# Kernel optimization log

Hardware: AMD Instinct MI355X
Metric: run time of the kernel (lower is better)

The kernel has to match this reference:

```python
import jax, jax.numpy as jnp
import numpy as np

TAU = 1.0
EPS = 1e-8  # F.cosine_similarity eps


def _cl(X, Y):
    # Pairwise cosine similarity via L2-normalize + single GEMM (N,D)@(D,N)
    Xn = X / jnp.maximum(jnp.linalg.norm(X, axis=1, keepdims=True), EPS)
    Yn = Y / jnp.maximum(jnp.linalg.norm(Y, axis=1, keepdims=True), EPS)
    sim = Xn @ Yn.T  # [N, N], sim[i, j] = cos(X_i, Y_j)
    e = jnp.exp(sim / TAU)
    pos = jnp.diagonal(e)               # exp(diag(sim)/tau), [N]
    neg = jnp.sum(e, axis=0) - pos      # column sums minus positive, [N]
    return -jnp.log(pos / neg).reshape(X.shape[0], 1)


def setup_inputs() -> dict:
    key = jax.random.key(0)
    ks = jax.random.split(key, 6)
    N, D1, D2, DO = 8192, 1024, 768, 256
    X = jax.random.normal(ks[0], (N, D1), dtype=jnp.float32)
    Y = jax.random.normal(ks[1], (N, D2), dtype=jnp.float32)
    # nn.Linear params (kaiming-uniform-ish scale)
    Wx = jax.random.uniform(ks[2], (DO, D1), jnp.float32, -1, 1) / np.sqrt(D1)
    bx = jax.random.uniform(ks[3], (DO,), jnp.float32, -1, 1) / np.sqrt(D1)
    Wy = jax.random.uniform(ks[4], (DO, D2), jnp.float32, -1, 1) / np.sqrt(D2)
    by = jax.random.uniform(ks[5], (DO,), jnp.float32, -1, 1) / np.sqrt(D2)
    return {"X": X, "Y": Y, "Wx": Wx, "bx": bx, "Wy": Wy, "by": by}


def reference(X, Y, Wx, bx, Wy, by):
    Xp = X @ Wx.T + bx  # proj_x
    Yp = Y @ Wy.T + by  # proj_y
    return _cl(Xp, Yp) + _cl(Yp, Xp)  # [N, 1]
```

## Files before the change

kernel.cpp:

```cpp
#include <hip/hip_runtime.h>
#include <hip/hip_bf16.h>

typedef __bf16 bf16_t;
typedef __bf16 bf16x8 __attribute__((ext_vector_type(8)));
typedef float  f32x4  __attribute__((ext_vector_type(4)));
typedef unsigned long u64;
typedef u64 u64x2 __attribute__((ext_vector_type(2)));

__device__ __forceinline__ bf16x8 pack8(f32x4 a, f32x4 b) {
    bf16x8 h = { (bf16_t)a.x, (bf16_t)a.y, (bf16_t)a.z, (bf16_t)a.w,
                 (bf16_t)b.x, (bf16_t)b.y, (bf16_t)b.z, (bf16_t)b.w };
    return h;
}

__device__ __forceinline__ void gl_lds16(const void* g, void* l) {
    __builtin_amdgcn_global_load_lds(
        (const __attribute__((address_space(1))) unsigned int*)g,
        (__attribute__((address_space(3))) unsigned int*)l, 16, 0, 0);
}

#if __has_builtin(__builtin_amdgcn_cvt_pk_fp8_f32)
__device__ __forceinline__ unsigned char cvt1_e4m3(float x) {
    return (unsigned char)(__builtin_amdgcn_cvt_pk_fp8_f32(x, x, 0, false) & 0xff);
}
#else
__device__ __forceinline__ unsigned char cvt1_e4m3(float x) {
    unsigned u = __float_as_uint(x);
    unsigned sign = (u >> 24) & 0x80u;
    float a = fabsf(x);
    if (a < 7.8125e-3f) { int q = (int)(a * 512.0f + 0.5f); return (unsigned char)(sign | q); }
    if (a >= 448.0f) return (unsigned char)(sign | 0x7E);
    unsigned au = u & 0x7FFFFFFFu;
    unsigned lsb = (au >> 20) & 1u;
    au += 0x7FFFFu + lsb;
    int exp = (int)(au >> 23) - 127;
    unsigned man = (au >> 20) & 7u;
    return (unsigned char)(sign | ((unsigned)(exp + 7) << 3) | man);
}
#endif

__device__ __forceinline__ int frag_off_k(int row16, int k) {
    return ((k >> 6) << 10) + (((k >> 3) & 3) << 8) + (row16 << 4)
         + (((k >> 5) & 1) << 3) + (k & 7);
}

__global__ __launch_bounds__(256) void wconv(
    const float* __restrict__ Wx, const float* __restrict__ Wy,
    bf16_t* __restrict__ Wxt, bf16_t* __restrict__ Wyt,
    float* __restrict__ sums)
{
    int id = blockIdx.x * 256 + threadIdx.x;
    if (blockIdx.x < 64) sums[id] = 0.0f;

    int row, k0, K;
    const float* W;
    bf16_t* Wt;
    if (id < 32768) { W = Wx; Wt = Wxt; K = 1024; row = id >> 7; k0 = (id & 127) << 3; }
    else { int c = id - 32768; W = Wy; Wt = Wyt; K = 768; row = c / 96; k0 = (c % 96) << 3; }

    f32x4 lo = *reinterpret_cast<const f32x4*>(&W[(size_t)row * K + k0]);
    f32x4 hi = *reinterpret_cast<const f32x4*>(&W[(size_t)row * K + k0 + 4]);
    size_t off = (size_t)(row >> 4) * 16 * K + frag_off_k(row & 15, k0);
    *reinterpret_cast<bf16x8*>(Wt + off) = pack8(lo, hi);
}

__global__ __launch_bounds__(512, 2) void proj_norm(
    const float* __restrict__ X, const float* __restrict__ Y,
    const bf16_t* __restrict__ Wxt, const float* __restrict__ bxp,
    const bf16_t* __restrict__ Wyt, const float* __restrict__ byp,
    unsigned char* __restrict__ Xt, unsigned char* __restrict__ Yt)
{
    __shared__ float Abuf[2][64 * 64];
    __shared__ unsigned char obuf[16384];
    __shared__ float ssq2[4][2][16];

    const int tid   = threadIdx.x;
    const int lane  = tid & 63;
    const int wave  = tid >> 6;
    const int quad  = lane >> 4;
    const int c16   = lane & 15;
    const int strip = wave >> 1;
    const int half  = wave & 1;

    const bool isY = blockIdx.x >= 128;
    const float*  A    = isY ? Y   : X;
    const bf16_t* Wt   = isY ? Wyt : Wxt;
    const float*  bias = isY ? byp : bxp;
    unsigned char* dst = isY ? Yt  : Xt;
    const int K = isY ? 768 : 1024;
    const int S = K >> 6;
    const int rowBase = (blockIdx.x & 127) * 64;

    auto stage = [&](int s, int b) {
        #pragma unroll
        for (int t = 0; t < 2; ++t) {
            int r0  = (wave * 2 + t) * 4;
            int row = r0 + (lane >> 4);
            int gch = (lane & 15) ^ (row & 15);
            gl_lds16(&A[(size_t)(rowBase + row) * K + s * 64 + gch * 4],
                     &Abuf[b][r0 * 64]);
        }
    };

    auto aFrag = [&](int b, int s2) -> bf16x8 {
        int row = strip * 16 + c16;
        int e   = s2 * 8 + quad * 2;
        const float* base = &Abuf[b][row * 64];
        f32x4 lo = *reinterpret_cast<const f32x4*>(base + ((e ^ c16) << 2));
        f32x4 hi = *reinterpret_cast<const f32x4*>(base + (((e + 1) ^ c16) << 2));
        return pack8(lo, hi);
    };

    const bf16_t* pB = Wt + (size_t)(half * 8) * 16 * K + quad * 256 + c16 * 16;
    const size_t tStride = (size_t)16 * K;

    f32x4 acc[8] = {};
    stage(0, 0);

    for (int s = 0; s < S; ++s) {
        const int b = s & 1;
        __syncthreads();
        if (s + 1 < S) stage(s + 1, b ^ 1);
        #pragma unroll
        for (int s2 = 0; s2 < 2; ++s2) {
            bf16x8 aF = aFrag(b, s2);
            #pragma unroll
            for (int nf = 0; nf < 8; ++nf) {
                bf16x8 bF = *reinterpret_cast<const bf16x8*>(
                    pB + (size_t)nf * tStride + s * 1024 + s2 * 8);
                acc[nf] = __builtin_amdgcn_mfma_f32_16x16x32_bf16(aF, bF, acc[nf], 0, 0, 0);
            }
        }
    }

    #pragma unroll
    for (int nf = 0; nf < 8; ++nf) {
        float bb = bias[half * 128 + nf * 16 + c16];
        #pragma unroll
        for (int r = 0; r < 4; ++r) acc[nf][r] += bb;
    }

    #pragma unroll
    for (int r = 0; r < 4; ++r) {
        float v = 0.f;
        #pragma unroll
        for (int nf = 0; nf < 8; ++nf) v += acc[nf][r] * acc[nf][r];
        v += __shfl_xor(v, 1, 64);
        v += __shfl_xor(v, 2, 64);
        v += __shfl_xor(v, 4, 64);
        v += __shfl_xor(v, 8, 64);
        if (c16 == 0) ssq2[strip][half][quad * 4 + r] = v;
    }
    __syncthreads();

    #pragma unroll
    for (int r = 0; r < 4; ++r) {
        int row16 = quad * 4 + r;
        float t = ssq2[strip][0][row16] + ssq2[strip][1][row16];
        float inv = 1.0f / fmaxf(sqrtf(t), 1e-8f);
        #pragma unroll
        for (int nf = 0; nf < 8; ++nf) {
            int k = half * 128 + nf * 16 + c16;
            obuf[strip * 4096 + frag_off_k(row16, k)] = cvt1_e4m3(acc[nf][r] * inv);
        }
    }
    __syncthreads();

    const f32x4* src = reinterpret_cast<const f32x4*>(&obuf[tid * 32]);
    f32x4* g = reinterpret_cast<f32x4*>(dst + (size_t)rowBase * 256 + tid * 32);
    g[0] = src[0];
    g[1] = src[1];
}

__global__ __launch_bounds__(256) void sim_gemm(
    const unsigned char* __restrict__ Xt, const unsigned char* __restrict__ Yt,
    float* __restrict__ rowsum, float* __restrict__ colsum,
    float* __restrict__ pos)
{
    __shared__ float red[256];

    const int tid  = threadIdx.x;
    const int lane = tid & 63;
    const int wave = tid >> 6;
    const int quad = lane >> 4;
    const int c16  = lane & 15;
    const int wy   = wave >> 1;
    const int wx   = wave & 1;
    const int rowBase = blockIdx.x * 128;
    const int colBase = blockIdx.y * 128;

    const u64x2* pa[4];
    const u64x2* pb[4];
    #pragma unroll
    for (int mf = 0; mf < 4; ++mf)
        pa[mf] = reinterpret_cast<const u64x2*>(
            Xt + (size_t)(rowBase + wy * 64 + mf * 16) * 256 + quad * 256 + c16 * 16);
    #pragma unroll
    for (int nf = 0; nf < 4; ++nf)
        pb[nf] = reinterpret_cast<const u64x2*>(
            Yt + (size_t)(colBase + wx * 64 + nf * 16) * 256 + quad * 256 + c16 * 16);

    f32x4 acc[4][4] = {};

    auto loadf = [&](u64x2* A, u64x2* B, int slab) {
        #pragma unroll
        for (int i = 0; i < 4; ++i) {
            A[i] = pa[i][slab * 64];
            B[i] = pb[i][slab * 64];
        }
    };
    auto mm = [&](const u64x2* A, const u64x2* B) {
        #pragma unroll
        for (int mf = 0; mf < 4; ++mf)
            #pragma unroll
            for (int nf = 0; nf < 4; ++nf)
                acc[mf][nf] = __builtin_amdgcn_mfma_f32_16x16x32_fp8_fp8(
                    (long)A[mf].x, (long)B[nf].x, acc[mf][nf], 0, 0, 0);
        #pragma unroll
        for (int mf = 0; mf < 4; ++mf)
            #pragma unroll
            for (int nf = 0; nf < 4; ++nf)
                acc[mf][nf] = __builtin_amdgcn_mfma_f32_16x16x32_fp8_fp8(
                    (long)A[mf].y, (long)B[nf].y, acc[mf][nf], 0, 0, 0);
    };

    u64x2 A0[4], B0[4], A1[4], B1[4];
    loadf(A0, B0, 0);
    loadf(A1, B1, 1);
    mm(A0, B0);
    loadf(A0, B0, 2);
    mm(A1, B1);
    loadf(A1, B1, 3);
    mm(A0, B0);
    mm(A1, B1);

    #pragma unroll
    for (int mf = 0; mf < 4; ++mf)
        #pragma unroll
        for (int nf = 0; nf < 4; ++nf)
            #pragma unroll
            for (int r = 0; r < 4; ++r)
                acc[mf][nf][r] = __expf(acc[mf][nf][r]);

    if (rowBase == colBase) {
        #pragma unroll
        for (int mf = 0; mf < 4; ++mf)
            #pragma unroll
            for (int nf = 0; nf < 4; ++nf)
                #pragma unroll
                for (int r = 0; r < 4; ++r) {
                    int lrow = wy * 64 + mf * 16 + quad * 4 + r;
                    int lcol = wx * 64 + nf * 16 + c16;
                    if (lrow == lcol) pos[rowBase + lrow] = acc[mf][nf][r];
                }
    }

    float rs[4][4];
    #pragma unroll
    for (int mf = 0; mf < 4; ++mf)
        #pragma unroll
        for (int r = 0; r < 4; ++r) {
            float v = acc[mf][0][r] + acc[mf][1][r] + acc[mf][2][r] + acc[mf][3][r];
            v += __shfl_xor(v, 1, 64);
            v += __shfl_xor(v, 2, 64);
            v += __shfl_xor(v, 4, 64);
            v += __shfl_xor(v, 8, 64);
            rs[mf][r] = v;
        }

    float cs[4];
    #pragma unroll
    for (int nf = 0; nf < 4; ++nf) {
        float v = 0.f;
        #pragma unroll
        for (int mf = 0; mf < 4; ++mf)
            #pragma unroll
            for (int r = 0; r < 4; ++r)
                v += acc[mf][nf][r];
        v += __shfl_xor(v, 16, 64);
        v += __shfl_xor(v, 32, 64);
        cs[nf] = v;
    }

    red[tid] = 0.f;
    __syncthreads();

    if (c16 == 0) {
        #pragma unroll
        for (int mf = 0; mf < 4; ++mf)
            #pragma unroll
            for (int r = 0; r < 4; ++r)
                atomicAdd(&red[wy * 64 + mf * 16 + quad * 4 + r], rs[mf][r]);
    }
    if (quad == 0) {
        #pragma unroll
        for (int nf = 0; nf < 4; ++nf)
            atomicAdd(&red[128 + wx * 64 + nf * 16 + c16], cs[nf]);
    }
    __syncthreads();

    if (tid < 128) atomicAdd(&rowsum[rowBase + tid], red[tid]);
    else           atomicAdd(&colsum[colBase + tid - 128], red[tid]);
}

__global__ __launch_bounds__(256) void finalize(
    const float* __restrict__ rowsum, const float* __restrict__ colsum,
    const float* __restrict__ pos, float* __restrict__ out)
{
    int i = blockIdx.x * 256 + threadIdx.x;
    float p = pos[i];
    out[i] = logf(colsum[i] - p) + logf(rowsum[i] - p) - 2.0f * logf(p);
}

extern "C" void kernel_launch(void* const* d_in, const int* in_sizes, int n_in,
                              void* d_out, int out_size, void* d_ws, size_t ws_size,
                              hipStream_t stream) {
    const float* X  = (const float*)d_in[0];
    const float* Y  = (const float*)d_in[1];
    const float* Wx = (const float*)d_in[2];
    const float* bx = (const float*)d_in[3];
    const float* Wy = (const float*)d_in[4];
    const float* by = (const float*)d_in[5];
    float* out = (float*)d_out;

    char* ws = (char*)d_ws;
    unsigned char* Xt  = (unsigned char*)(ws);
    unsigned char* Yt  = (unsigned char*)(ws + (2u << 20));
    bf16_t*        Wxt = (bf16_t*)(ws + (4u << 20));
    bf16_t*        Wyt = (bf16_t*)(ws + (4u << 20) + (512u << 10));
    float* rowsum = (float*)(ws + (5u << 20));
    float* colsum = rowsum + 8192;
    float* pos    = colsum + 8192;

    wconv<<<224, 256, 0, stream>>>(Wx, Wy, Wxt, Wyt, rowsum);
    proj_norm<<<256, 512, 0, stream>>>(X, Y, Wxt, bx, Wyt, by, Xt, Yt);
    sim_gemm<<<dim3(64, 64), 256, 0, stream>>>(Xt, Yt, rowsum, colsum, pos);
    finalize<<<32, 256, 0, stream>>>(rowsum, colsum, pos, out);
}
```

Measured before the change: 168.1 us.

## Retile projection waves 2x4 and stage shared X tiles through LDS in sim GEMM

The projection kernel now splits its 8 waves as 2 row groups by 4 column groups, so each wave computes 32 rows by 64 columns. B fragments are loaded once per k-step and reused across two A fragments, which reduces global weight reads per wave. The row-norm reduction now combines partial sums from four column groups. In the similarity GEMM, the A (Xt) operand is staged into double-buffered LDS with global_load_lds and shared by the waves that need the same rows, instead of each wave reading from global memory. This adds __syncthreads barriers per slab, which could limit the overlap of loads with MFMA work.

```diff
diff --git a/kernel.cpp b/kernel.cpp
--- a/kernel.cpp
+++ b/kernel.cpp
@@ -72,15 +72,15 @@
 {
     __shared__ float Abuf[2][64 * 64];
     __shared__ unsigned char obuf[16384];
-    __shared__ float ssq2[4][2][16];
-
-    const int tid   = threadIdx.x;
-    const int lane  = tid & 63;
-    const int wave  = tid >> 6;
-    const int quad  = lane >> 4;
-    const int c16   = lane & 15;
-    const int strip = wave >> 1;
-    const int half  = wave & 1;
+    __shared__ float ssqL[4][64];
+
+    const int tid  = threadIdx.x;
+    const int lane = tid & 63;
+    const int wave = tid >> 6;
+    const int quad = lane >> 4;
+    const int c16  = lane & 15;
+    const int rg   = wave >> 2;
+    const int cg   = wave & 3;
 
     const bool isY = blockIdx.x >= 128;
     const float*  A    = isY ? Y   : X;
@@ -102,8 +102,8 @@
         }
     };
 
-    auto aFrag = [&](int b, int s2) -> bf16x8 {
-        int row = strip * 16 + c16;
+    auto aFrag = [&](int b, int mf, int s2) -> bf16x8 {
+        int row = rg * 32 + mf * 16 + c16;
         int e   = s2 * 8 + quad * 2;
         const float* base = &Abuf[b][row * 64];
         f32x4 lo = *reinterpret_cast<const f32x4*>(base + ((e ^ c16) << 2));
@@ -111,10 +111,12 @@
         return pack8(lo, hi);
     };
 
-    const bf16_t* pB = Wt + (size_t)(half * 8) * 16 * K + quad * 256 + c16 * 16;
-    const size_t tStride = (size_t)16 * K;
-
-    f32x4 acc[8] = {};
+    const bf16_t* pB[4];
+    #pragma unroll
+    for (int nf = 0; nf < 4; ++nf)
+        pB[nf] = Wt + (size_t)(cg * 4 + nf) * 16 * K + quad * 256 + c16 * 16;
+
+    f32x4 acc[2][4] = {};
     stage(0, 0);
 
     for (int s = 0; s < S; ++s) {
@@ -123,47 +125,59 @@
         if (s + 1 < S) stage(s + 1, b ^ 1);
         #pragma unroll
         for (int s2 = 0; s2 < 2; ++s2) {
-            bf16x8 aF = aFrag(b, s2);
-            #pragma unroll
-            for (int nf = 0; nf < 8; ++nf) {
-                bf16x8 bF = *reinterpret_cast<const bf16x8*>(
-                    pB + (size_t)nf * tStride + s * 1024 + s2 * 8);
-                acc[nf] = __builtin_amdgcn_mfma_f32_16x16x32_bf16(aF, bF, acc[nf], 0, 0, 0);
+            bf16x8 bF[4];
+            #pragma unroll
+            for (int nf = 0; nf < 4; ++nf)
+                bF[nf] = *reinterpret_cast<const bf16x8*>(pB[nf] + s * 1024 + s2 * 8);
+            #pragma unroll
+            for (int mf = 0; mf < 2; ++mf) {
+                bf16x8 aF = aFrag(b, mf, s2);
+                #pragma unroll
+                for (int nf = 0; nf < 4; ++nf)
+                    acc[mf][nf] = __builtin_amdgcn_mfma_f32_16x16x32_bf16(
+                        aF, bF[nf], acc[mf][nf], 0, 0, 0);
             }
         }
     }
 
     #pragma unroll
-    for (int nf = 0; nf < 8; ++nf) {
-        float bb = bias[half * 128 + nf * 16 + c16];
-        #pragma unroll
-        for (int r = 0; r < 4; ++r) acc[nf][r] += bb;
-    }
-
-    #pragma unroll
-    for (int r = 0; r < 4; ++r) {
-        float v = 0.f;
-        #pragma unroll
-        for (int nf = 0; nf < 8; ++nf) v += acc[nf][r] * acc[nf][r];
-        v += __shfl_xor(v, 1, 64);
-        v += __shfl_xor(v, 2, 64);
-        v += __shfl_xor(v, 4, 64);
-        v += __shfl_xor(v, 8, 64);
-        if (c16 == 0) ssq2[strip][half][quad * 4 + r] = v;
-    }
-    __syncthreads();
-
-    #pragma unroll
-    for (int r = 0; r < 4; ++r) {
-        int row16 = quad * 4 + r;
-        float t = ssq2[strip][0][row16] + ssq2[strip][1][row16];
-        float inv = 1.0f / fmaxf(sqrtf(t), 1e-8f);
-        #pragma unroll
-        for (int nf = 0; nf < 8; ++nf) {
-            int k = half * 128 + nf * 16 + c16;
-            obuf[strip * 4096 + frag_off_k(row16, k)] = cvt1_e4m3(acc[nf][r] * inv);
-        }
-    }
+    for (int nf = 0; nf < 4; ++nf) {
+        float bb = bias[cg * 64 + nf * 16 + c16];
+        #pragma unroll
+        for (int mf = 0; mf < 2; ++mf)
+            #pragma unroll
+            for (int r = 0; r < 4; ++r) acc[mf][nf][r] += bb;
+    }
+
+    #pragma unroll
+    for (int mf = 0; mf < 2; ++mf)
+        #pragma unroll
+        for (int r = 0; r < 4; ++r) {
+            float v = 0.f;
+            #pragma unroll
+            for (int nf = 0; nf < 4; ++nf) v += acc[mf][nf][r] * acc[mf][nf][r];
+            v += __shfl_xor(v, 1, 64);
+            v += __shfl_xor(v, 2, 64);
+            v += __shfl_xor(v, 4, 64);
+            v += __shfl_xor(v, 8, 64);
+            if (c16 == 0) ssqL[cg][rg * 32 + mf * 16 + quad * 4 + r] = v;
+        }
+    __syncthreads();
+
+    #pragma unroll
+    for (int mf = 0; mf < 2; ++mf)
+        #pragma unroll
+        for (int r = 0; r < 4; ++r) {
+            int lr = rg * 32 + mf * 16 + quad * 4 + r;
+            float t = ssqL[0][lr] + ssqL[1][lr] + ssqL[2][lr] + ssqL[3][lr];
+            float inv = 1.0f / fmaxf(sqrtf(t), 1e-8f);
+            #pragma unroll
+            for (int nf = 0; nf < 4; ++nf) {
+                int k = cg * 64 + nf * 16 + c16;
+                obuf[((lr >> 4) << 12) + frag_off_k(lr & 15, k)] =
+                    cvt1_e4m3(acc[mf][nf][r] * inv);
+            }
+        }
     __syncthreads();
 
     const f32x4* src = reinterpret_cast<const f32x4*>(&obuf[tid * 32]);
@@ -177,6 +191,7 @@
     float* __restrict__ rowsum, float* __restrict__ colsum,
     float* __restrict__ pos)
 {
+    __shared__ unsigned char As[2][8192];
     __shared__ float red[256];
 
     const int tid  = threadIdx.x;
@@ -189,12 +204,16 @@
     const int rowBase = blockIdx.x * 128;
     const int colBase = blockIdx.y * 128;
 
-    const u64x2* pa[4];
+    auto stageA = [&](int s, int b) {
+        #pragma unroll
+        for (int t = 0; t < 2; ++t) {
+            int tile = wave * 2 + t;
+            gl_lds16(Xt + (((size_t)(blockIdx.x * 8 + tile)) << 12) + s * 1024 + lane * 16,
+                     &As[b][tile << 10]);
+        }
+    };
+
     const u64x2* pb[4];
-    #pragma unroll
-    for (int mf = 0; mf < 4; ++mf)
-        pa[mf] = reinterpret_cast<const u64x2*>(
-            Xt + (size_t)(rowBase + wy * 64 + mf * 16) * 256 + quad * 256 + c16 * 16);
     #pragma unroll
     for (int nf = 0; nf < 4; ++nf)
         pb[nf] = reinterpret_cast<const u64x2*>(
@@ -202,12 +221,15 @@
 
     f32x4 acc[4][4] = {};
 
-    auto loadf = [&](u64x2* A, u64x2* B, int slab) {
-        #pragma unroll
-        for (int i = 0; i < 4; ++i) {
-            A[i] = pa[i][slab * 64];
-            B[i] = pb[i][slab * 64];
-        }
+    auto loadA = [&](u64x2* A, int b) {
+        #pragma unroll
+        for (int mf = 0; mf < 4; ++mf)
+            A[mf] = *reinterpret_cast<const u64x2*>(
+                &As[b][((wy * 4 + mf) << 10) + quad * 256 + c16 * 16]);
+    };
+    auto loadB = [&](u64x2* B, int slab) {
+        #pragma unroll
+        for (int nf = 0; nf < 4; ++nf) B[nf] = pb[nf][slab * 64];
     };
     auto mm = [&](const u64x2* A, const u64x2* B) {
         #pragma unroll
@@ -224,15 +246,27 @@
                     (long)A[mf].y, (long)B[nf].y, acc[mf][nf], 0, 0, 0);
     };
 
-    u64x2 A0[4], B0[4], A1[4], B1[4];
-    loadf(A0, B0, 0);
-    loadf(A1, B1, 1);
-    mm(A0, B0);
-    loadf(A0, B0, 2);
-    mm(A1, B1);
-    loadf(A1, B1, 3);
-    mm(A0, B0);
-    mm(A1, B1);
+    u64x2 Af[4], B0[4], B1[4];
+    stageA(0, 0);
+    loadB(B0, 0);
+    __syncthreads();
+    stageA(1, 1);
+    loadB(B1, 1);
+    loadA(Af, 0);
+    mm(Af, B0);
+    __syncthreads();
+    stageA(2, 0);
+    loadB(B0, 2);
+    loadA(Af, 1);
+    mm(Af, B1);
+    __syncthreads();
+    stageA(3, 1);
+    loadB(B1, 3);
+    loadA(Af, 0);
+    mm(Af, B0);
+    __syncthreads();
+    loadA(Af, 1);
+    mm(Af, B1);
 
     #pragma unroll
     for (int mf = 0; mf < 4; ++mf)
```

After: 168.7 us. Within noise of the previous version (+0.4%).

## Halve proj_norm row tile to 32 rows and split columns across four waves

Applied to the files above, without the earlier changes.

The projection+normalize kernel now handles 32 rows per block instead of 64, launching 512 blocks rather than 256. Waves are rearranged into 2 row groups by 4 column groups of 64 output columns each, so each wave holds four accumulators instead of eight. Per-row sums of squares are reduced across four column-group partials. The aim is to fill more of the GPU's CUs and raise occupancy, since 256 blocks underfill the MI355X. The cost is that each block reads the full weight matrix for fewer rows, doubling weight-fragment global reads.

```diff
diff --git a/kernel.cpp b/kernel.cpp
--- a/kernel.cpp
+++ b/kernel.cpp
@@ -64,46 +64,43 @@
     *reinterpret_cast<bf16x8*>(Wt + off) = pack8(lo, hi);
 }
 
-__global__ __launch_bounds__(512, 2) void proj_norm(
+__global__ __launch_bounds__(512, 4) void proj_norm(
     const float* __restrict__ X, const float* __restrict__ Y,
     const bf16_t* __restrict__ Wxt, const float* __restrict__ bxp,
     const bf16_t* __restrict__ Wyt, const float* __restrict__ byp,
     unsigned char* __restrict__ Xt, unsigned char* __restrict__ Yt)
 {
-    __shared__ float Abuf[2][64 * 64];
-    __shared__ unsigned char obuf[16384];
-    __shared__ float ssq2[4][2][16];
-
-    const int tid   = threadIdx.x;
-    const int lane  = tid & 63;
-    const int wave  = tid >> 6;
-    const int quad  = lane >> 4;
-    const int c16   = lane & 15;
-    const int strip = wave >> 1;
-    const int half  = wave & 1;
-
-    const bool isY = blockIdx.x >= 128;
+    __shared__ float Abuf[2][32 * 64];
+    __shared__ unsigned char obuf[8192];
+    __shared__ float ssqL[4][32];
+
+    const int tid  = threadIdx.x;
+    const int lane = tid & 63;
+    const int wave = tid >> 6;
+    const int quad = lane >> 4;
+    const int c16  = lane & 15;
+    const int rg   = wave >> 2;
+    const int cg   = wave & 3;
+
+    const bool isY = blockIdx.x >= 256;
     const float*  A    = isY ? Y   : X;
     const bf16_t* Wt   = isY ? Wyt : Wxt;
     const float*  bias = isY ? byp : bxp;
     unsigned char* dst = isY ? Yt  : Xt;
     const int K = isY ? 768 : 1024;
     const int S = K >> 6;
-    const int rowBase = (blockIdx.x & 127) * 64;
+    const int rowBase = (blockIdx.x & 255) * 32;
 
     auto stage = [&](int s, int b) {
-        #pragma unroll
-        for (int t = 0; t < 2; ++t) {
-            int r0  = (wave * 2 + t) * 4;
-            int row = r0 + (lane >> 4);
-            int gch = (lane & 15) ^ (row & 15);
-            gl_lds16(&A[(size_t)(rowBase + row) * K + s * 64 + gch * 4],
-                     &Abuf[b][r0 * 64]);
-        }
+        int r0  = wave * 4;
+        int row = r0 + (lane >> 4);
+        int gch = (lane & 15) ^ (row & 15);
+        gl_lds16(&A[(size_t)(rowBase + row) * K + s * 64 + gch * 4],
+                 &Abuf[b][r0 * 64]);
     };
 
     auto aFrag = [&](int b, int s2) -> bf16x8 {
-        int row = strip * 16 + c16;
+        int row = rg * 16 + c16;
         int e   = s2 * 8 + quad * 2;
         const float* base = &Abuf[b][row * 64];
         f32x4 lo = *reinterpret_cast<const f32x4*>(base + ((e ^ c16) << 2));
@@ -111,10 +108,12 @@
         return pack8(lo, hi);
     };
 
-    const bf16_t* pB = Wt + (size_t)(half * 8) * 16 * K + quad * 256 + c16 * 16;
-    const size_t tStride = (size_t)16 * K;
-
-    f32x4 acc[8] = {};
+    const bf16_t* pB[4];
+    #pragma unroll
+    for (int nf = 0; nf < 4; ++nf)
+        pB[nf] = Wt + (size_t)(cg * 4 + nf) * 16 * K + quad * 256 + c16 * 16;
+
+    f32x4 acc[4] = {};
     stage(0, 0);
 
     for (int s = 0; s < S; ++s) {
@@ -125,17 +124,16 @@
         for (int s2 = 0; s2 < 2; ++s2) {
             bf16x8 aF = aFrag(b, s2);
             #pragma unroll
-            for (int nf = 0; nf < 8; ++nf) {
-                bf16x8 bF = *reinterpret_cast<const bf16x8*>(
-                    pB + (size_t)nf * tStride + s * 1024 + s2 * 8);
+            for (int nf = 0; nf < 4; ++nf) {
+                bf16x8 bF = *reinterpret_cast<const bf16x8*>(pB[nf] + s * 1024 + s2 * 8);
                 acc[nf] = __builtin_amdgcn_mfma_f32_16x16x32_bf16(aF, bF, acc[nf], 0, 0, 0);
             }
         }
     }
 
     #pragma unroll
-    for (int nf = 0; nf < 8; ++nf) {
-        float bb = bias[half * 128 + nf * 16 + c16];
+    for (int nf = 0; nf < 4; ++nf) {
+        float bb = bias[cg * 64 + nf * 16 + c16];
         #pragma unroll
         for (int r = 0; r < 4; ++r) acc[nf][r] += bb;
     }
@@ -144,32 +142,32 @@
     for (int r = 0; r < 4; ++r) {
         float v = 0.f;
         #pragma unroll
-        for (int nf = 0; nf < 8; ++nf) v += acc[nf][r] * acc[nf][r];
+        for (int nf = 0; nf < 4; ++nf) v += acc[nf][r] * acc[nf][r];
         v += __shfl_xor(v, 1, 64);
         v += __shfl_xor(v, 2, 64);
         v += __shfl_xor(v, 4, 64);
         v += __shfl_xor(v, 8, 64);
-        if (c16 == 0) ssq2[strip][half][quad * 4 + r] = v;
+        if (c16 == 0) ssqL[cg][rg * 16 + quad * 4 + r] = v;
     }
     __syncthreads();
 
     #pragma unroll
     for (int r = 0; r < 4; ++r) {
-        int row16 = quad * 4 + r;
-        float t = ssq2[strip][0][row16] + ssq2[strip][1][row16];
+        int lr = rg * 16 + quad * 4 + r;
+        float t = ssqL[0][lr] + ssqL[1][lr] + ssqL[2][lr] + ssqL[3][lr];
         float inv = 1.0f / fmaxf(sqrtf(t), 1e-8f);
         #pragma unroll
-        for (int nf = 0; nf < 8; ++nf) {
-            int k = half * 128 + nf * 16 + c16;
-            obuf[strip * 4096 + frag_off_k(row16, k)] = cvt1_e4m3(acc[nf][r] * inv);
+        for (int nf = 0; nf < 4; ++nf) {
+            int k = cg * 64 + nf * 16 + c16;
+            obuf[((lr >> 4) << 12) + frag_off_k(lr & 15, k)] =
+                cvt1_e4m3(acc[nf][r] * inv);
         }
     }
     __syncthreads();
 
-    const f32x4* src = reinterpret_cast<const f32x4*>(&obuf[tid * 32]);
-    f32x4* g = reinterpret_cast<f32x4*>(dst + (size_t)rowBase * 256 + tid * 32);
+    const f32x4* src = reinterpret_cast<const f32x4*>(&obuf[tid * 16]);
+    f32x4* g = reinterpret_cast<f32x4*>(dst + (size_t)rowBase * 256 + tid * 16);
     g[0] = src[0];
-    g[1] = src[1];
 }
 
 __global__ __launch_bounds__(256) void sim_gemm(
@@ -333,7 +331,7 @@
     float* pos    = colsum + 8192;
 
     wconv<<<224, 256, 0, stream>>>(Wx, Wy, Wxt, Wyt, rowsum);
-    proj_norm<<<256, 512, 0, stream>>>(X, Y, Wxt, bx, Wyt, by, Xt, Yt);
+    proj_norm<<<512, 512, 0, stream>>>(X, Y, Wxt, bx, Wyt, by, Xt, Yt);
     sim_gemm<<<dim3(64, 64), 256, 0, stream>>>(Xt, Yt, rowsum, colsum, pos);
     finalize<<<32, 256, 0, stream>>>(rowsum, colsum, pos, out);
 }
```

Result: slower. 172.1 us (+2.3%).
